# Optimization experiments

Measured on AMD Instinct MI355X. Metric: run time of the kernel, lower is better.

Reference implementation:

```python
import jax, jax.numpy as jnp
import numpy as np

B, T, INPUT_SIZE = 64, 1024, 128
RESERVOIR_SIZE, OUTPUT_SIZE = 2048, 256


def setup_inputs() -> dict:
    key = jax.random.key(0)
    ks = jax.random.split(key, 7)
    s_in = 1.0 / np.sqrt(INPUT_SIZE)
    s_res = 1.0 / np.sqrt(RESERVOIR_SIZE)
    return {
        "input": jax.random.normal(ks[0], (B, T, INPUT_SIZE), dtype=jnp.float32),
        # PyTorch Linear weights: [out_features, in_features]
        "W_in_w": jax.random.uniform(ks[1], (RESERVOIR_SIZE, INPUT_SIZE), jnp.float32, -s_in, s_in),
        "W_in_b": jax.random.uniform(ks[2], (RESERVOIR_SIZE,), jnp.float32, -s_in, s_in),
        "W_res_w": jax.random.uniform(ks[3], (RESERVOIR_SIZE, RESERVOIR_SIZE), jnp.float32, -s_res, s_res),
        "W_res_b": jax.random.uniform(ks[4], (RESERVOIR_SIZE,), jnp.float32, -s_res, s_res),
        "W_out_w": jax.random.uniform(ks[5], (OUTPUT_SIZE, RESERVOIR_SIZE), jnp.float32, -s_res, s_res),
        "W_out_b": jax.random.uniform(ks[6], (OUTPUT_SIZE,), jnp.float32, -s_res, s_res),
    }


def reference(input, W_in_w, W_in_b, W_res_w, W_res_b, W_out_w, W_out_b):
    # Precompute input projections for all timesteps: [T, B, R]
    xin = jnp.einsum('bti,ri->tbr', input, W_in_w) + W_in_b

    def step(h, x_t):
        h_new = jnp.tanh(x_t + h @ W_res_w.T + W_res_b)
        return h_new, None

    h0 = jnp.zeros((input.shape[0], W_res_w.shape[0]), dtype=input.dtype)
    h_final, _ = jax.lax.scan(step, h0, xin)
    # Output readout: [B, output_size]
    return h_final @ W_out_w.T + W_out_b
```

## Files before the change

### kernel.cpp

```cpp
#include <hip/hip_runtime.h>
#include <hip/hip_bf16.h>
#include <cstdint>

#define B_ 64
#define T_ 1024
#define I_ 128
#define R_ 2048
#define O_ 256
#define NBLK 256
#define NSLOT 65
#define SLOTB 32768
#define RSTRIDE (NSLOT * SLOTB)

typedef __attribute__((ext_vector_type(8))) __bf16 bf16x8;
typedef __attribute__((ext_vector_type(4))) float f32x4;
typedef __attribute__((ext_vector_type(4))) unsigned int u32x4;
typedef unsigned short u16;
typedef unsigned int u32;
typedef unsigned long long u64;

#define AT_LDR(p) __hip_atomic_load((p), __ATOMIC_RELAXED, __HIP_MEMORY_SCOPE_AGENT)

__device__ __forceinline__ u16 f2bf(float f) {
    u32 u = __builtin_bit_cast(u32, f);
    u32 r = (u + 0x7FFFu + ((u >> 16) & 1u)) >> 16;
    return (u16)r;
}

__device__ __forceinline__ bf16x8 cvt8r(f32x4 a, f32x4 b) {
    union { u16 h[8]; bf16x8 v; } u;
    u.h[0] = f2bf(a[0]); u.h[1] = f2bf(a[1]); u.h[2] = f2bf(a[2]); u.h[3] = f2bf(a[3]);
    u.h[4] = f2bf(b[0]); u.h[5] = f2bf(b[1]); u.h[6] = f2bf(b[2]); u.h[7] = f2bf(b[3]);
    return u.v;
}

__device__ __forceinline__ bf16x8 ldbf8(const u16* p) {
    return *reinterpret_cast<const bf16x8*>(p);
}

__device__ __forceinline__ u32 sentchk(bf16x8 v) {
    u32x4 u = __builtin_bit_cast(u32x4, v);
    u32 b = 0;
    #pragma unroll
    for (int k = 0; k < 4; ++k) {
        b |= (u32)((u[k] >> 16) == 0x7FC0u);
        b |= (u32)((u[k] & 0xFFFFu) == 0x7FC0u);
    }
    return b;
}


__global__ void conv_bf16_kernel(const float* __restrict__ src,
                                 u16* __restrict__ dst, int n) {
    int stride = gridDim.x * blockDim.x;
    for (int i = blockIdx.x * blockDim.x + threadIdx.x; i < n; i += stride)
        dst[i] = f2bf(src[i]);
}

__global__ void bias_sum_kernel(const float* __restrict__ a,
                                const float* __restrict__ b,
                                float* __restrict__ c, int n) {
    int i = blockIdx.x * blockDim.x + threadIdx.x;
    if (i < n) c[i] = a[i] + b[i];
}

__global__ void ring_init_kernel(u32* __restrict__ ring) {
    const int perg = NSLOT * (SLOTB / 4);
    const int total = 8 * perg;
    int stride = gridDim.x * blockDim.x;
    for (int idx = blockIdx.x * blockDim.x + threadIdx.x; idx < total; idx += stride) {
        int within = idx % perg;
        int slot = within / (SLOTB / 4);
        ring[idx] = slot ? 0x7FC07FC0u : 0u;
    }
}

__global__ __launch_bounds__(512, 2) void esn_persist(
    const u16* __restrict__ Wrb, const u16* __restrict__ Wib,
    const float* __restrict__ input, const float* __restrict__ bias,
    u16* __restrict__ ring, const u16* __restrict__ zpage,
    u32* __restrict__ cnt, u16* __restrict__ hfinal)
{
    __shared__ char wlds[65536];
    __shared__ f32x4 red[8][4][64];
    __shared__ u16 xout[8][64];
    __shared__ int s_grp, s_ns, s_mode;

    const int tid  = threadIdx.x;
    const int lane = tid & 63;
    const int w    = tid >> 6;
    const int lcol = lane & 15;
    const int lkh  = lane >> 4;
    const int arow = lcol;

    if (tid == 0) {
        u32 xcd;
        asm volatile("s_getreg_b32 %0, hwreg(20, 0, 32)" : "=s"(xcd));
        xcd &= 7;
        int slotA = (int)__hip_atomic_fetch_add(&cnt[xcd], 1u, __ATOMIC_RELAXED,
                                                __HIP_MEMORY_SCOPE_AGENT);
        int gslot = (int)__hip_atomic_fetch_add(&cnt[8], 1u, __ATOMIC_ACQ_REL,
                                                __HIP_MEMORY_SCOPE_AGENT);
        while (AT_LDR(&cnt[8]) < 256u) { }
        u32 c[8], tot;
        do {
            tot = 0;
            #pragma unroll
            for (int i = 0; i < 8; ++i) { c[i] = AT_LDR(&cnt[i]); tot += c[i]; }
        } while (tot != 256u);
        int bal = 1;
        #pragma unroll
        for (int i = 0; i < 8; ++i) bal &= (c[i] == 32u);
        s_mode = bal;
        s_grp  = bal ? (int)xcd : (gslot >> 5);
        s_ns   = bal ? (slotA & 31) : (gslot & 31);
    }
    __syncthreads();
    const int grp = s_grp;
    const int ns  = s_ns;
    bool ic = (s_mode == 0);

    {
        const u16* bp0 = Wrb + (size_t)(ns * 64 + lcol) * R_ + w * 256 + lkh * 8;
        #pragma unroll
        for (int j = 0; j < 8; ++j) {
            *reinterpret_cast<bf16x8*>(wlds + ((size_t)(w * 8 + j) * 64 + lane) * 16)
                = ldbf8(bp0 + j * 32);
        }
    }
    bf16x8 wf1[8], wf2[8], wf3[8];
    {
        const u16* bp1 = Wrb + (size_t)(ns * 64 + 16 + lcol) * R_ + w * 256 + lkh * 8;
        const u16* bp2 = Wrb + (size_t)(ns * 64 + 32 + lcol) * R_ + w * 256 + lkh * 8;
        const u16* bp3 = Wrb + (size_t)(ns * 64 + 48 + lcol) * R_ + w * 256 + lkh * 8;
        #define WL(dst, bp, OFF) \
            asm volatile("global_load_dwordx4 %0, %1, off offset:" OFF \
                         : "=v"(dst) : "v"(bp))
        WL(wf1[0], bp1, "0");   WL(wf1[1], bp1, "64");  WL(wf1[2], bp1, "128");
        WL(wf1[3], bp1, "192"); WL(wf1[4], bp1, "256"); WL(wf1[5], bp1, "320");
        WL(wf1[6], bp1, "384"); WL(wf1[7], bp1, "448");
        WL(wf2[0], bp2, "0");   WL(wf2[1], bp2, "64");  WL(wf2[2], bp2, "128");
        WL(wf2[3], bp2, "192"); WL(wf2[4], bp2, "256"); WL(wf2[5], bp2, "320");
        WL(wf2[6], bp2, "384"); WL(wf2[7], bp2, "448");
        WL(wf3[0], bp3, "0");   WL(wf3[1], bp3, "64");  WL(wf3[2], bp3, "128");
        WL(wf3[3], bp3, "192"); WL(wf3[4], bp3, "256"); WL(wf3[5], bp3, "320");
        WL(wf3[6], bp3, "384"); WL(wf3[7], bp3, "448");
        #undef WL
    }
    bf16x8 wi[4];
    float bs = 0.f;
    if (w < 4) {
        const u16* wp = Wib + (size_t)(ns * 64 + w * 16 + lcol) * I_ + lkh * 8;
        asm volatile("global_load_dwordx4 %0, %1, off"            : "=v"(wi[0]) : "v"(wp));
        asm volatile("global_load_dwordx4 %0, %1, off offset:64"  : "=v"(wi[1]) : "v"(wp));
        asm volatile("global_load_dwordx4 %0, %1, off offset:128" : "=v"(wi[2]) : "v"(wp));
        asm volatile("global_load_dwordx4 %0, %1, off offset:192" : "=v"(wi[3]) : "v"(wp));
        bs = bias[ns * 64 + w * 16 + lcol];
    }
    asm volatile("s_waitcnt vmcnt(0)" ::: "memory");
    __builtin_amdgcn_sched_barrier(0);

    char* ringB = (char*)ring + (size_t)grp * RSTRIDE;
    const char* zb = (const char*)zpage;
    const float* xrow = input + (size_t)(grp * 8 + (arow & 7)) * T_ * I_;
    const char* wl0 = wlds + ((size_t)w * 8 * 64 + lane) * 16;

    #define LOAD8(F)                                                          \
        asm volatile(                                                         \
            "global_load_dwordx4 %0, %8, off " F "\n\t"                       \
            "global_load_dwordx4 %1, %8, off offset:64 " F "\n\t"             \
            "global_load_dwordx4 %2, %8, off offset:128 " F "\n\t"            \
            "global_load_dwordx4 %3, %8, off offset:192 " F "\n\t"            \
            "global_load_dwordx4 %4, %8, off offset:256 " F "\n\t"            \
            "global_load_dwordx4 %5, %8, off offset:320 " F "\n\t"            \
            "global_load_dwordx4 %6, %8, off offset:384 " F "\n\t"            \
            "global_load_dwordx4 %7, %8, off offset:448 " F "\n\t"            \
            "s_waitcnt vmcnt(0)"                                              \
            : "=&v"(h0), "=&v"(h1), "=&v"(h2), "=&v"(h3),                     \
              "=&v"(h4), "=&v"(h5), "=&v"(h6), "=&v"(h7)                      \
            : "v"(Ah)                                                         \
            : "memory")

    int rs = 0;
    for (int t = 0; t < T_; ++t) {
        const int wsl = (rs + 1 == NSLOT) ? 0 : rs + 1;
        const int ps  = (rs == 0) ? NSLOT - 1 : rs - 1;
        const char* slotR = ringB + (size_t)rs  * SLOTB;
        char*       slotW = ringB + (size_t)wsl * SLOTB;
        char*       slotP = ringB + (size_t)ps  * SLOTB;

        f32x4 facc = {0.f, 0.f, 0.f, 0.f};
        if (w < 4) {
            const float* Ax = xrow + (size_t)t * I_ + lkh * 8;
            const f32x4 z4 = {0.f, 0.f, 0.f, 0.f};
            #pragma unroll
            for (int kc = 0; kc < 4; ++kc) {
                f32x4 xa = z4, xb = z4;
                if (arow < 8) {
                    xa = *reinterpret_cast<const f32x4*>(Ax + kc * 32);
                    xb = *reinterpret_cast<const f32x4*>(Ax + kc * 32 + 4);
                }
                facc = __builtin_amdgcn_mfma_f32_16x16x32_bf16(cvt8r(xa, xb), wi[kc], facc, 0, 0, 0);
            }
        }

        const char* base = (arow < 8) ? (slotR + arow * 4096) : zb;
        const char* Ah = base + (size_t)(w * 256 + lkh * 8) * 2;
        bf16x8 h0, h1, h2, h3, h4, h5, h6, h7;
        {
            u32 bad; int anybad; int spins = 0;
            do {
                if (ic) { LOAD8("sc1"); } else { LOAD8("sc0"); }
                __builtin_amdgcn_sched_barrier(0);
                bad = sentchk(h0) | sentchk(h1) | sentchk(h2) | sentchk(h3) |
                      sentchk(h4) | sentchk(h5) | sentchk(h6) | sentchk(h7);
                anybad = __any((int)bad);
                if (anybad && !ic && ++spins >= 64) ic = true;
            } while (anybad);
        }

        f32x4 acc0 = {0.f,0.f,0.f,0.f}, acc1 = {0.f,0.f,0.f,0.f};
        f32x4 acc2 = {0.f,0.f,0.f,0.f}, acc3 = {0.f,0.f,0.f,0.f};
        #define RSTEP(J, HJ)                                                      \
        {                                                                         \
            bf16x8 b0 = *reinterpret_cast<const bf16x8*>(wl0 + (J) * 1024);       \
            acc0 = __builtin_amdgcn_mfma_f32_16x16x32_bf16(HJ, b0,      acc0, 0, 0, 0); \
            acc1 = __builtin_amdgcn_mfma_f32_16x16x32_bf16(HJ, wf1[J],  acc1, 0, 0, 0); \
            acc2 = __builtin_amdgcn_mfma_f32_16x16x32_bf16(HJ, wf2[J],  acc2, 0, 0, 0); \
            acc3 = __builtin_amdgcn_mfma_f32_16x16x32_bf16(HJ, wf3[J],  acc3, 0, 0, 0); \
        }
        RSTEP(0, h0) RSTEP(1, h1) RSTEP(2, h2) RSTEP(3, h3)
        RSTEP(4, h4) RSTEP(5, h5) RSTEP(6, h6) RSTEP(7, h7)
        #undef RSTEP

        red[w][0][lane] = acc0;
        red[w][1][lane] = acc1;
        red[w][2][lane] = acc2;
        red[w][3][lane] = acc3;
        __syncthreads();

        if (w < 4) {
            f32x4 tot = red[0][w][lane];
            #pragma unroll
            for (int ww = 1; ww < 8; ++ww) tot += red[ww][w][lane];
            tot += facc;
            #pragma unroll
            for (int i = 0; i < 4; ++i) {
                int orow = lkh * 4 + i;
                if (orow < 8)
                    xout[orow][w * 16 + lcol] = f2bf(tanhf(tot[i] + bs));
            }
        }
        __syncthreads();

        if (w == 0) {
            bf16x8 v = ldbf8(&xout[lane >> 3][(lane & 7) * 8]);
            char* dst = slotW + (size_t)(lane >> 3) * 4096 + ns * 128 + (lane & 7) * 16;
            asm volatile("global_store_dwordx4 %0, %1, off sc1"
                         :: "v"(dst), "v"(v) : "memory");
        }
        if (w == 1) {
            u32x4 sq = {0x7FC07FC0u, 0x7FC07FC0u, 0x7FC07FC0u, 0x7FC07FC0u};
            char* dst = slotP + (size_t)(lane >> 3) * 4096 + ns * 128 + (lane & 7) * 16;
            asm volatile("global_store_dwordx4 %0, %1, off sc1"
                         :: "v"(dst), "v"(sq) : "memory");
        }
        if (w == 2 && t == T_ - 1) {
            bf16x8 v = ldbf8(&xout[lane >> 3][(lane & 7) * 8]);
            *reinterpret_cast<bf16x8*>(
                hfinal + (size_t)(grp * 8 + (lane >> 3)) * R_ + ns * 64 + (lane & 7) * 8) = v;
        }
        rs = wsl;
    }
    #undef LOAD8
}

__global__ __launch_bounds__(128) void readout_kernel(
    const u16* __restrict__ h, const u16* __restrict__ Wo,
    const float* __restrict__ b_out, float* __restrict__ out)
{
    const int lane = threadIdx.x & 63;
    const int wid  = threadIdx.x >> 6;
    const int g    = blockIdx.x * 2 + wid;
    const int m    = g >> 4;
    const int n    = g & 15;
    const int koff = (lane >> 4) * 8;
    const int b    = m * 16 + (lane & 15);
    const int col  = n * 16 + (lane & 15);

    f32x4 acc0 = {0.f,0.f,0.f,0.f};
    f32x4 acc1 = {0.f,0.f,0.f,0.f};
    f32x4 acc2 = {0.f,0.f,0.f,0.f};
    f32x4 acc3 = {0.f,0.f,0.f,0.f};

    const u16* Ah = h + (size_t)b * R_ + koff;
    const u16* Bh = Wo + (size_t)col * R_ + koff;
    #pragma unroll 4
    for (int kc = 0; kc < 64; kc += 4) {
        acc0 = __builtin_amdgcn_mfma_f32_16x16x32_bf16(ldbf8(Ah + (kc + 0) * 32), ldbf8(Bh + (kc + 0) * 32), acc0, 0, 0, 0);
        acc1 = __builtin_amdgcn_mfma_f32_16x16x32_bf16(ldbf8(Ah + (kc + 1) * 32), ldbf8(Bh + (kc + 1) * 32), acc1, 0, 0, 0);
        acc2 = __builtin_amdgcn_mfma_f32_16x16x32_bf16(ldbf8(Ah + (kc + 2) * 32), ldbf8(Bh + (kc + 2) * 32), acc2, 0, 0, 0);
        acc3 = __builtin_amdgcn_mfma_f32_16x16x32_bf16(ldbf8(Ah + (kc + 3) * 32), ldbf8(Bh + (kc + 3) * 32), acc3, 0, 0, 0);
    }

    f32x4 s = acc0 + acc1 + acc2 + acc3;
    const float bo = b_out[col];
    #pragma unroll
    for (int i2 = 0; i2 < 4; ++i2) {
        int row = m * 16 + (lane >> 4) * 4 + i2;
        out[(size_t)row * O_ + col] = s[i2] + bo;
    }
}


extern "C" void kernel_launch(void* const* d_in, const int* in_sizes, int n_in,
                              void* d_out, int out_size, void* d_ws, size_t ws_size,
                              hipStream_t stream) {
    const float* in    = (const float*)d_in[0];
    const float* Winw  = (const float*)d_in[1];
    const float* Winb  = (const float*)d_in[2];
    const float* Wresw = (const float*)d_in[3];
    const float* Wresb = (const float*)d_in[4];
    const float* Woutw = (const float*)d_in[5];
    const float* Woutb = (const float*)d_in[6];
    float* out = (float*)d_out;

    char* ws = (char*)d_ws;
    u16*   Wrb    = (u16*)(ws);
    u16*   Wib    = (u16*)(ws + 8388608);
    u16*   Wob    = (u16*)(ws + 8912896);
    float* bias   = (float*)(ws + 9961472);
    u16*   hfinal = (u16*)(ws + 9969664);
    u16*   zpage  = (u16*)(ws + 10231808);
    u32*   cnt    = (u32*)(ws + 10235904);
    u16*   ring   = (u16*)(ws + 10235968);

    conv_bf16_kernel<<<2048, 256, 0, stream>>>(Wresw, Wrb, R_ * R_);
    conv_bf16_kernel<<<256, 256, 0, stream>>>(Winw, Wib, R_ * I_);
    conv_bf16_kernel<<<512, 256, 0, stream>>>(Woutw, Wob, O_ * R_);
    bias_sum_kernel<<<8, 256, 0, stream>>>(Winb, Wresb, bias, R_);
    ring_init_kernel<<<4096, 256, 0, stream>>>((u32*)ring);
    hipMemsetAsync(zpage, 0, 4096 + 64, stream);

    esn_persist<<<NBLK, 512, 0, stream>>>(Wrb, Wib, in, bias,
                                          ring, zpage, cnt, hfinal);

    readout_kernel<<<32, 128, 0, stream>>>(hfinal, Wob, Woutb, out);
}
```

Baseline: 4.899 ms.

## Replace NaN-sentinel polling of ring data with per-slot canary flag polling

Before, each wave spun on 8 vector loads of the hidden-state ring slot and checked every element for a NaN sentinel. It also had to write sentinels back over the previous slot each step. Now each producer block stores its data, waits for the store to complete, then sets a per-slot dword flag, and consumers poll a small 16-byte flag vector before doing a single data load. This cuts the polling bandwidth, the sentinel compare work and the full-slot sentinel rewrite, and the ring init now only zeroes slot 0. In exchange it relies on data-then-flag store ordering being visible across blocks, and it adds one store-wait on the producer's critical path.

```diff
diff --git a/kernel.cpp b/kernel.cpp
--- a/kernel.cpp
+++ b/kernel.cpp
@@ -38,17 +38,6 @@
     return *reinterpret_cast<const bf16x8*>(p);
 }
 
-__device__ __forceinline__ u32 sentchk(bf16x8 v) {
-    u32x4 u = __builtin_bit_cast(u32x4, v);
-    u32 b = 0;
-    #pragma unroll
-    for (int k = 0; k < 4; ++k) {
-        b |= (u32)((u[k] >> 16) == 0x7FC0u);
-        b |= (u32)((u[k] & 0xFFFFu) == 0x7FC0u);
-    }
-    return b;
-}
-
 
 __global__ void conv_bf16_kernel(const float* __restrict__ src,
                                  u16* __restrict__ dst, int n) {
@@ -64,21 +53,25 @@
     if (i < n) c[i] = a[i] + b[i];
 }
 
-__global__ void ring_init_kernel(u32* __restrict__ ring) {
-    const int perg = NSLOT * (SLOTB / 4);
-    const int total = 8 * perg;
+__global__ void ring_init_kernel(u32* __restrict__ ring, u32* __restrict__ canary) {
+    int tid0 = blockIdx.x * blockDim.x + threadIdx.x;
     int stride = gridDim.x * blockDim.x;
-    for (int idx = blockIdx.x * blockDim.x + threadIdx.x; idx < total; idx += stride) {
-        int within = idx % perg;
-        int slot = within / (SLOTB / 4);
-        ring[idx] = slot ? 0x7FC07FC0u : 0u;
+    const int dcount = 8 * (SLOTB / 4);
+    for (int i = tid0; i < dcount; i += stride) {
+        int g = i / (SLOTB / 4), off = i % (SLOTB / 4);
+        ring[(size_t)g * (RSTRIDE / 4) + off] = 0;
+    }
+    const int ccount = 8 * NSLOT * 32;
+    for (int i = tid0; i < ccount; i += stride) {
+        int slot = (i >> 5) % NSLOT;
+        canary[i] = (slot == 0) ? 1u : 0u;
     }
 }
 
 __global__ __launch_bounds__(512, 2) void esn_persist(
     const u16* __restrict__ Wrb, const u16* __restrict__ Wib,
     const float* __restrict__ input, const float* __restrict__ bias,
-    u16* __restrict__ ring, const u16* __restrict__ zpage,
+    u16* __restrict__ ring, u32* __restrict__ canary,
     u32* __restrict__ cnt, u16* __restrict__ hfinal)
 {
     __shared__ char wlds[65536];
@@ -118,7 +111,8 @@
     __syncthreads();
     const int grp = s_grp;
     const int ns  = s_ns;
-    bool ic = (s_mode == 0);
+    const bool icD = (s_mode == 0);
+    bool ic = icD;
 
     {
         const u16* bp0 = Wrb + (size_t)(ns * 64 + lcol) * R_ + w * 256 + lkh * 8;
@@ -161,7 +155,7 @@
     __builtin_amdgcn_sched_barrier(0);
 
     char* ringB = (char*)ring + (size_t)grp * RSTRIDE;
-    const char* zb = (const char*)zpage;
+    u32*  canaryG = canary + (size_t)grp * (NSLOT * 32);
     const float* xrow = input + (size_t)(grp * 8 + (arow & 7)) * T_ * I_;
     const char* wl0 = wlds + ((size_t)w * 8 * 64 + lane) * 16;
 
@@ -187,7 +181,6 @@
         const int ps  = (rs == 0) ? NSLOT - 1 : rs - 1;
         const char* slotR = ringB + (size_t)rs  * SLOTB;
         char*       slotW = ringB + (size_t)wsl * SLOTB;
-        char*       slotP = ringB + (size_t)ps  * SLOTB;
 
         f32x4 facc = {0.f, 0.f, 0.f, 0.f};
         if (w < 4) {
@@ -204,19 +197,35 @@
             }
         }
 
-        const char* base = (arow < 8) ? (slotR + arow * 4096) : zb;
-        const char* Ah = base + (size_t)(w * 256 + lkh * 8) * 2;
+        {
+            const u32* cp = canaryG + (size_t)rs * 32 + (w << 2);
+            u32x4 cv;
+            int spins = 0;
+            for (;;) {
+                if (ic) {
+                    asm volatile("global_load_dwordx4 %0, %1, off sc1\n\t"
+                                 "s_waitcnt vmcnt(0)"
+                                 : "=v"(cv) : "v"(cp) : "memory");
+                } else {
+                    asm volatile("global_load_dwordx4 %0, %1, off sc0\n\t"
+                                 "s_waitcnt vmcnt(0)"
+                                 : "=v"(cv) : "v"(cp) : "memory");
+                }
+                if ((cv[0] & cv[1] & cv[2] & cv[3]) == 1u) break;
+                if (!ic && ++spins >= 64) ic = true;
+            }
+            __builtin_amdgcn_sched_barrier(0);
+        }
+
         bf16x8 h0, h1, h2, h3, h4, h5, h6, h7;
         {
-            u32 bad; int anybad; int spins = 0;
-            do {
-                if (ic) { LOAD8("sc1"); } else { LOAD8("sc0"); }
-                __builtin_amdgcn_sched_barrier(0);
-                bad = sentchk(h0) | sentchk(h1) | sentchk(h2) | sentchk(h3) |
-                      sentchk(h4) | sentchk(h5) | sentchk(h6) | sentchk(h7);
-                anybad = __any((int)bad);
-                if (anybad && !ic && ++spins >= 64) ic = true;
-            } while (anybad);
+            const u32x4 zz = {0u, 0u, 0u, 0u};
+            h0 = __builtin_bit_cast(bf16x8, zz); h1 = h0; h2 = h0; h3 = h0;
+            h4 = h0; h5 = h0; h6 = h0; h7 = h0;
+            if (arow < 8) {
+                const char* Ah = slotR + (size_t)arow * 4096 + (size_t)(w * 256 + lkh * 8) * 2;
+                if (icD) { LOAD8("sc1"); } else { LOAD8("sc0"); }
+            }
         }
 
         f32x4 acc0 = {0.f,0.f,0.f,0.f}, acc1 = {0.f,0.f,0.f,0.f};
@@ -258,12 +267,19 @@
             char* dst = slotW + (size_t)(lane >> 3) * 4096 + ns * 128 + (lane & 7) * 16;
             asm volatile("global_store_dwordx4 %0, %1, off sc1"
                          :: "v"(dst), "v"(v) : "memory");
-        }
-        if (w == 1) {
-            u32x4 sq = {0x7FC07FC0u, 0x7FC07FC0u, 0x7FC07FC0u, 0x7FC07FC0u};
-            char* dst = slotP + (size_t)(lane >> 3) * 4096 + ns * 128 + (lane & 7) * 16;
-            asm volatile("global_store_dwordx4 %0, %1, off sc1"
-                         :: "v"(dst), "v"(sq) : "memory");
+            asm volatile("s_waitcnt vmcnt(0)" ::: "memory");
+            if (lane == 0) {
+                u32 one = 1u;
+                u32* cd = canaryG + (size_t)wsl * 32 + ns;
+                asm volatile("global_store_dword %0, %1, off sc1"
+                             :: "v"(cd), "v"(one) : "memory");
+            }
+        }
+        if (w == 1 && lane == 0) {
+            u32 zero = 0u;
+            u32* cd = canaryG + (size_t)ps * 32 + ns;
+            asm volatile("global_store_dword %0, %1, off sc1"
+                         :: "v"(cd), "v"(zero) : "memory");
         }
         if (w == 2 && t == T_ - 1) {
             bf16x8 v = ldbf8(&xout[lane >> 3][(lane & 7) * 8]);
@@ -331,19 +347,19 @@
     u16*   Wob    = (u16*)(ws + 8912896);
     float* bias   = (float*)(ws + 9961472);
     u16*   hfinal = (u16*)(ws + 9969664);
-    u16*   zpage  = (u16*)(ws + 10231808);
-    u32*   cnt    = (u32*)(ws + 10235904);
-    u16*   ring   = (u16*)(ws + 10235968);
+    u32*   canary = (u32*)(ws + 10231808);
+    u32*   cnt    = (u32*)(ws + 10298368);
+    u16*   ring   = (u16*)(ws + 10298432);
 
     conv_bf16_kernel<<<2048, 256, 0, stream>>>(Wresw, Wrb, R_ * R_);
     conv_bf16_kernel<<<256, 256, 0, stream>>>(Winw, Wib, R_ * I_);
     conv_bf16_kernel<<<512, 256, 0, stream>>>(Woutw, Wob, O_ * R_);
     bias_sum_kernel<<<8, 256, 0, stream>>>(Winb, Wresb, bias, R_);
-    ring_init_kernel<<<4096, 256, 0, stream>>>((u32*)ring);
-    hipMemsetAsync(zpage, 0, 4096 + 64, stream);
+    ring_init_kernel<<<1024, 256, 0, stream>>>((u32*)ring, canary);
+    hipMemsetAsync(cnt, 0, 64, stream);
 
     esn_persist<<<NBLK, 512, 0, stream>>>(Wrb, Wib, in, bias,
-                                          ring, zpage, cnt, hfinal);
+                                          ring, canary, cnt, hfinal);
 
     readout_kernel<<<32, 128, 0, stream>>>(hfinal, Wob, Woutb, out);
 }
```

After: 7.775 ms. 1.59x slower.
